# Optimization experiments

Measured on AMD Instinct MI355X. Metric: run time of the kernel, lower is better.

## Reference

```python
import jax, jax.numpy as jnp
import numpy as np

N_NODES = 100000
N_EDGES = 1600000
N_GRAPHS = 256
IN_C = 64
C = 128
N_LAYERS = 5
LN_EPS = 1e-5


def setup_inputs() -> dict:
    key = jax.random.key(0)
    ks = jax.random.split(key, 16)
    x = jax.random.normal(ks[0], (N_NODES, IN_C), dtype=jnp.float32)
    edge_index = jax.random.randint(ks[1], (2, N_EDGES), 0, N_NODES, dtype=jnp.int32)
    batch = jnp.sort(jax.random.randint(ks[2], (N_NODES,), 0, N_GRAPHS, dtype=jnp.int32))
    s_in = 1.0 / np.sqrt(IN_C)
    s_c = 1.0 / np.sqrt(C)
    s_2c = 1.0 / np.sqrt(2 * C)
    return {
        "x": x,
        "edge_index": edge_index,
        "batch": batch,
        "proj_w": jax.random.uniform(ks[3], (IN_C, C), jnp.float32, -s_in, s_in),
        "proj_b": jax.random.uniform(ks[4], (C,), jnp.float32, -s_in, s_in),
        "gin_w1": jax.random.uniform(ks[5], (N_LAYERS, C, C), jnp.float32, -s_c, s_c),
        "gin_b1": jax.random.uniform(ks[6], (N_LAYERS, C), jnp.float32, -s_c, s_c),
        "gin_w2": jax.random.uniform(ks[7], (N_LAYERS, C, C), jnp.float32, -s_c, s_c),
        "gin_b2": jax.random.uniform(ks[8], (N_LAYERS, C), jnp.float32, -s_c, s_c),
        "ln_g": jnp.ones((N_LAYERS, C), jnp.float32),
        "ln_b": jnp.zeros((N_LAYERS, C), jnp.float32),
        "fw1": jax.random.uniform(ks[9], (C, 2 * C), jnp.float32, -s_c, s_c),
        "fb1": jax.random.uniform(ks[10], (2 * C,), jnp.float32, -s_c, s_c),
        "fw2": jax.random.uniform(ks[11], (2 * C, C), jnp.float32, -s_2c, s_2c),
        "fb2": jax.random.uniform(ks[12], (C,), jnp.float32, -s_2c, s_2c),
    }


def _layer_norm(h, g, b):
    mu = jnp.mean(h, axis=-1, keepdims=True)
    var = jnp.mean(jnp.square(h - mu), axis=-1, keepdims=True)
    return (h - mu) * jax.lax.rsqrt(var + LN_EPS) * g + b


def reference(x, edge_index, batch, proj_w, proj_b, gin_w1, gin_b1, gin_w2, gin_b2,
              ln_g, ln_b, fw1, fb1, fw2, fb2):
    src, dst = edge_index[0], edge_index[1]
    h = x @ proj_w + proj_b  # [N, C]
    for i in range(N_LAYERS):
        # GINConv (eps=0): mlp(x_i + sum_{j in N(i)} x_j)
        aggr = jax.ops.segment_sum(h[src], dst, num_segments=N_NODES)  # [N, C]
        z = h + aggr
        z = jax.nn.relu(z @ gin_w1[i] + gin_b1[i]) @ gin_w2[i] + gin_b2[i]
        h = _layer_norm(jax.nn.relu(z), ln_g[i], ln_b[i])
    # global add pool over graphs
    g = jax.ops.segment_sum(h, batch, num_segments=N_GRAPHS)  # [G, C]
    out = jax.nn.relu(g @ fw1 + fb1) @ fw2 + fb2  # [G, C]
    return out
```

## Files before the change

kernel.cpp:

```cpp
#include <hip/hip_runtime.h>
#include <hip/hip_bf16.h>

#define N_NODES  100000
#define N_EDGES  1600000
#define N_GRAPHS 256
#define CCH      128
#define INC      64
#define N_LAYERS 5
#define SLICE_N  12500
#define POOL_SPLIT 16
#define CAP_A    16
#define CAP_B    32
#define CAP      (CAP_A + CAP_B)

typedef __attribute__((ext_vector_type(8))) short  short8;
typedef __attribute__((ext_vector_type(4))) float  f32x4;

__device__ __forceinline__ float bits2f(unsigned int u){ union{unsigned int i; float f;} v; v.i=u; return v.f; }
__device__ __forceinline__ float b2f(unsigned short u){ return bits2f(((unsigned int)u)<<16); }
__device__ __forceinline__ float lo16(unsigned int u){ return bits2f(u<<16); }
__device__ __forceinline__ float hi16(unsigned int u){ return bits2f(u & 0xffff0000u); }
__device__ __forceinline__ unsigned short f2b(float f){
  union{float f; unsigned int i;} v; v.f=f;
  unsigned int r = v.i + 0x7fffu + ((v.i>>16)&1u);
  return (unsigned short)(r>>16);
}
#define ACC8(a, r) { a[0]+=lo16(r.x); a[1]+=hi16(r.x); a[2]+=lo16(r.y); a[3]+=hi16(r.y); \
                     a[4]+=lo16(r.z); a[5]+=hi16(r.z); a[6]+=lo16(r.w); a[7]+=hi16(r.w); }

__global__ void pack_kernel(const float* __restrict__ projw,
                            const float* __restrict__ w1,
                            const float* __restrict__ w2,
                            unsigned short* __restrict__ wp)
{
  int idx = blockIdx.x*256 + threadIdx.x;
  const float* src; int rem;
  if (idx < 8192) { src = projw; rem = idx; }
  else {
    int t2 = idx - 8192;
    int mat = t2 >> 14;
    rem = t2 & 16383;
    src = (mat < 5) ? (w1 + mat*16384) : (w2 + (mat-5)*16384);
  }
  int f    = rem >> 9;
  int lane = (rem >> 3) & 63;
  int j    = rem & 7;
  int kk = f >> 3, nn = f & 7;
  int k = kk*32 + (lane>>4)*8 + j;
  int n = nn*16 + (lane&15);
  wp[idx] = f2b(src[k*CCH + n]);
}

__global__ __launch_bounds__(256) void fill_kernel(const int* __restrict__ src, const int* __restrict__ dst,
                                                   int* __restrict__ cnt,
                                                   int* __restrict__ esrcA, int* __restrict__ esrcB){
  int slice = blockIdx.x & 7;
  int lo = slice * SLICE_N, hi = lo + SLICE_N;
  int stride = (gridDim.x >> 3) * 256;
  for (int e = (blockIdx.x>>3)*256 + threadIdx.x; e < N_EDGES; e += stride){
    int d = __builtin_nontemporal_load(&dst[e]);
    if (d >= lo && d < hi){
      int s = __builtin_nontemporal_load(&src[e]);
      int p = atomicAdd(&cnt[d], 1);
      if (p < CAP_A)      esrcA[(size_t)d*CAP_A + p] = s;
      else if (p < CAP)   esrcB[(size_t)d*CAP_B + (p - CAP_A)] = s;
    }
  }
}

__global__ void bsearch_kernel(const int* __restrict__ batch, int* __restrict__ gstart){
  int g = threadIdx.x;
  int lo = 0, hi = N_NODES;
  while (lo < hi){
    int mid = (lo + hi) >> 1;
    if (batch[mid] < g) lo = mid + 1; else hi = mid;
  }
  gstart[g] = lo;
  if (g == 255) gstart[256] = N_NODES;
}

__global__ __launch_bounds__(256) void aggr_kernel(const unsigned short* __restrict__ h,
                                                   const int* __restrict__ cnt,
                                                   const int* __restrict__ esrcA,
                                                   const int* __restrict__ esrcB,
                                                   unsigned short* __restrict__ z)
{
  int node = blockIdx.x*4 + (threadIdx.x>>6);
  int lane = threadIdx.x & 63;
  int s = lane >> 4, c = lane & 15;
  const uint4* h16 = (const uint4*)h;
  float a[8];
  if (s == 0){
    uint4 v = h16[(size_t)node*16 + c];
    a[0]=lo16(v.x); a[1]=hi16(v.x); a[2]=lo16(v.y); a[3]=hi16(v.y);
    a[4]=lo16(v.z); a[5]=hi16(v.z); a[6]=lo16(v.w); a[7]=hi16(v.w);
  } else {
    #pragma unroll
    for (int k=0;k<8;k++) a[k] = 0.f;
  }
  int n = cnt[node]; if (n > CAP) n = CAP;
  const int* epA = esrcA + (size_t)node*CAP_A;
  const int* epB = esrcB + (size_t)node*CAP_B;

  int e = s;
  uint4 r0, r1;
  bool p0 = e < n;
  bool p1 = (e + 4) < n;
  if (p0){
    int sn = (e < CAP_A) ? epA[e] : epB[e - CAP_A];
    r0 = h16[(size_t)sn*16 + c];
  }
  if (p1){
    int e1 = e + 4;
    int sn = (e1 < CAP_A) ? epA[e1] : epB[e1 - CAP_A];
    r1 = h16[(size_t)sn*16 + c];
  }
  while (p0){
    uint4 r2; bool p2 = (e + 8) < n;
    if (p2){
      int e2 = e + 8;
      int sn = (e2 < CAP_A) ? epA[e2] : epB[e2 - CAP_A];
      r2 = h16[(size_t)sn*16 + c];
    }
    ACC8(a, r0);
    r0 = r1; p0 = p1;
    r1 = r2; p1 = p2;
    e += 4;
  }

  #pragma unroll
  for (int k=0;k<8;k++){
    a[k] += __shfl_xor(a[k], 16, 64);
    a[k] += __shfl_xor(a[k], 32, 64);
  }
  if (s == 0){
    uint4 o;
    o.x = (unsigned int)f2b(a[0]) | ((unsigned int)f2b(a[1])<<16);
    o.y = (unsigned int)f2b(a[2]) | ((unsigned int)f2b(a[3])<<16);
    o.z = (unsigned int)f2b(a[4]) | ((unsigned int)f2b(a[5])<<16);
    o.w = (unsigned int)f2b(a[6]) | ((unsigned int)f2b(a[7])<<16);
    ((uint4*)z)[(size_t)node*16 + c] = o;
  }
}

__global__ __launch_bounds__(256) void projgemm_kernel(
    const float* __restrict__ X,
    const unsigned short* __restrict__ Wp,
    const float* __restrict__ bias,
    unsigned short* __restrict__ out,
    int M)
{
  const int tid = threadIdx.x;
  const int wave = tid>>6, lane = tid&63;
  const int rbase = blockIdx.x*128 + wave*32;
  if (rbase >= M) return;
  const int cl = lane & 15, rg = lane >> 4;
  const bool ok1 = (rbase + 16) < M;

  f32x4 acc[2][8];
  #pragma unroll
  for (int s=0;s<2;s++)
    #pragma unroll
    for (int nn=0;nn<8;nn++) acc[s][nn] = (f32x4){0.f,0.f,0.f,0.f};

  const short8* wp8 = (const short8*)Wp;
  #pragma unroll
  for (int kk=0;kk<2;kk++){
    short8 bfr[8];
    #pragma unroll
    for (int nn=0;nn<8;nn++) bfr[nn] = wp8[(kk*8+nn)*64 + lane];
    #pragma unroll
    for (int s=0;s<2;s++){
      if (s==1 && !ok1) break;
      const float* xp = X + (size_t)(rbase + s*16 + cl)*INC + kk*32 + rg*8;
      float4 v0 = *(const float4*)xp;
      float4 v1 = *(const float4*)(xp+4);
      short8 af;
      af[0]=(short)f2b(v0.x); af[1]=(short)f2b(v0.y); af[2]=(short)f2b(v0.z); af[3]=(short)f2b(v0.w);
      af[4]=(short)f2b(v1.x); af[5]=(short)f2b(v1.y); af[6]=(short)f2b(v1.z); af[7]=(short)f2b(v1.w);
      #pragma unroll
      for (int nn=0;nn<8;nn++)
        acc[s][nn] = __builtin_amdgcn_mfma_f32_16x16x32_bf16(af, bfr[nn], acc[s][nn],0,0,0);
    }
  }

  float bc[8];
  #pragma unroll
  for (int nn=0;nn<8;nn++) bc[nn] = bias[nn*16+cl];

  #pragma unroll
  for (int s=0;s<2;s++){
    if (s==1 && !ok1) break;
    const int rowb = rbase + s*16 + rg*4;
    #pragma unroll
    for (int j=0;j<4;j++){
      unsigned short* op = out + (size_t)(rowb+j)*CCH + cl;
      #pragma unroll
      for (int nn=0;nn<8;nn++) op[nn*16] = f2b(acc[s][nn][j] + bc[nn]);
    }
  }
}

__global__ __launch_bounds__(256) void gemm12_kernel(
    const unsigned short* __restrict__ A,
    const unsigned short* __restrict__ Wp1,
    const float* __restrict__ b1,
    const unsigned short* __restrict__ Wp2,
    const float* __restrict__ b2,
    const float* __restrict__ lng,
    const float* __restrict__ lnb,
    unsigned short* __restrict__ out, int M)
{
  __shared__ unsigned short tl[4][32][136];
  const int tid = threadIdx.x;
  const int wave = tid>>6, lane = tid&63;
  const int rbase = blockIdx.x*128 + wave*32;
  if (rbase >= M) return;
  const int cl = lane & 15, rg = lane >> 4;
  const bool ok1 = (rbase + 16) < M;

  {
    f32x4 acc[2][8];
    #pragma unroll
    for (int s=0;s<2;s++)
      #pragma unroll
      for (int nn=0;nn<8;nn++) acc[s][nn] = (f32x4){0.f,0.f,0.f,0.f};

    const short8* wp8 = (const short8*)Wp1;
    #pragma unroll
    for (int kk=0;kk<4;kk++){
      short8 bfr[8];
      #pragma unroll
      for (int nn=0;nn<8;nn++) bfr[nn] = wp8[(kk*8+nn)*64 + lane];
      const unsigned short* ap = A + (size_t)(rbase+cl)*CCH + kk*32 + rg*8;
      short8 a0 = *(const short8*)ap;
      #pragma unroll
      for (int nn=0;nn<8;nn++)
        acc[0][nn] = __builtin_amdgcn_mfma_f32_16x16x32_bf16(a0, bfr[nn], acc[0][nn],0,0,0);
      if (ok1){
        short8 a1 = *(const short8*)(ap + (size_t)16*CCH);
        #pragma unroll
        for (int nn=0;nn<8;nn++)
          acc[1][nn] = __builtin_amdgcn_mfma_f32_16x16x32_bf16(a1, bfr[nn], acc[1][nn],0,0,0);
      }
    }
    float bc[8];
    #pragma unroll
    for (int nn=0;nn<8;nn++) bc[nn] = b1[nn*16+cl];
    #pragma unroll
    for (int s=0;s<2;s++){
      if (s==1 && !ok1) break;
      #pragma unroll
      for (int j=0;j<4;j++){
        int rel = s*16 + rg*4 + j;
        #pragma unroll
        for (int nn=0;nn<8;nn++){
          float t = acc[s][nn][j] + bc[nn];
          tl[wave][rel][nn*16+cl] = f2b(fmaxf(t, 0.f));
        }
      }
    }
  }
  {
    f32x4 acc[2][8];
    #pragma unroll
    for (int s=0;s<2;s++)
      #pragma unroll
      for (int nn=0;nn<8;nn++) acc[s][nn] = (f32x4){0.f,0.f,0.f,0.f};

    const short8* wp8 = (const short8*)Wp2;
    #pragma unroll
    for (int kk=0;kk<4;kk++){
      short8 bfr[8];
      #pragma unroll
      for (int nn=0;nn<8;nn++) bfr[nn] = wp8[(kk*8+nn)*64 + lane];
      short8 a0 = *(const short8*)&tl[wave][cl][kk*32 + rg*8];
      #pragma unroll
      for (int nn=0;nn<8;nn++)
        acc[0][nn] = __builtin_amdgcn_mfma_f32_16x16x32_bf16(a0, bfr[nn], acc[0][nn],0,0,0);
      if (ok1){
        short8 a1 = *(const short8*)&tl[wave][16+cl][kk*32 + rg*8];
        #pragma unroll
        for (int nn=0;nn<8;nn++)
          acc[1][nn] = __builtin_amdgcn_mfma_f32_16x16x32_bf16(a1, bfr[nn], acc[1][nn],0,0,0);
      }
    }
    float bc[8], gg[8], bb[8];
    #pragma unroll
    for (int nn=0;nn<8;nn++){
      bc[nn] = b2[nn*16+cl];
      gg[nn] = lng[nn*16+cl];
      bb[nn] = lnb[nn*16+cl];
    }
    #pragma unroll
    for (int s=0;s<2;s++){
      if (s==1 && !ok1) break;
      float v[8][4];
      #pragma unroll
      for (int nn=0;nn<8;nn++)
        #pragma unroll
        for (int j=0;j<4;j++)
          v[nn][j] = fmaxf(acc[s][nn][j] + bc[nn], 0.f);
      #pragma unroll
      for (int j=0;j<4;j++){
        float sm=0.f, sq=0.f;
        #pragma unroll
        for (int nn=0;nn<8;nn++){ sm += v[nn][j]; sq += v[nn][j]*v[nn][j]; }
        #pragma unroll
        for (int m=1;m<16;m<<=1){ sm += __shfl_xor(sm, m, 64); sq += __shfl_xor(sq, m, 64); }
        float mean = sm * (1.f/128.f);
        float var  = fmaxf(sq * (1.f/128.f) - mean*mean, 0.f);
        float rs = rsqrtf(var + 1e-5f);
        #pragma unroll
        for (int nn=0;nn<8;nn++) v[nn][j] = (v[nn][j]-mean)*rs*gg[nn] + bb[nn];
      }
      const int rowb = rbase + s*16 + rg*4;
      #pragma unroll
      for (int j=0;j<4;j++){
        unsigned short* op = out + (size_t)(rowb+j)*CCH + cl;
        #pragma unroll
        for (int nn=0;nn<8;nn++) op[nn*16] = f2b(v[nn][j]);
      }
    }
  }
}

__global__ __launch_bounds__(64) void pool1_kernel(const unsigned short* __restrict__ h,
                                                   const int* __restrict__ gstart,
                                                   float* __restrict__ gpart)
{
  int g = blockIdx.x >> 4;
  int sp = blockIdx.x & 15;
  int lane = threadIdx.x;
  int n0 = gstart[g], n1 = gstart[g+1];
  const unsigned int* hu = (const unsigned int*)h;
  float a0 = 0.f, a1 = 0.f;
  for (int n = n0 + sp; n < n1; n += POOL_SPLIT){
    unsigned int v = hu[(size_t)n*64 + lane];
    a0 += lo16(v); a1 += hi16(v);
  }
  float2* gp = (float2*)gpart;
  gp[(size_t)blockIdx.x*64 + lane] = make_float2(a0, a1);
}

__global__ __launch_bounds__(64) void pool2_kernel(const float* __restrict__ gpart,
                                                   float* __restrict__ gout)
{
  int g = blockIdx.x;
  int lane = threadIdx.x;
  const float2* gp = (const float2*)gpart;
  float a0 = 0.f, a1 = 0.f;
  #pragma unroll
  for (int sp=0; sp<POOL_SPLIT; sp++){
    float2 v = gp[((size_t)g*POOL_SPLIT + sp)*64 + lane];
    a0 += v.x; a1 += v.y;
  }
  ((float2*)gout)[(size_t)g*64 + lane] = make_float2(a0, a1);
}

__global__ __launch_bounds__(256) void final_kernel(const float* __restrict__ gout,
                                                    const float* __restrict__ fw1,
                                                    const float* __restrict__ fb1,
                                                    const float* __restrict__ fw2,
                                                    const float* __restrict__ fb2,
                                                    float* __restrict__ out)
{
  __shared__ float gr[128];
  __shared__ float hid[256];
  int g = blockIdx.x, t = threadIdx.x;
  if (t < 128) gr[t] = gout[g*CCH + t];
  __syncthreads();
  float a = 0.f;
  for (int k=0;k<128;k++) a += gr[k] * fw1[k*256 + t];
  a += fb1[t];
  hid[t] = fmaxf(a, 0.f);
  __syncthreads();
  if (t < 128){
    float o = 0.f;
    for (int j=0;j<256;j++) o += hid[j] * fw2[j*128 + t];
    o += fb2[t];
    out[(size_t)g*CCH + t] = o;
  }
}

extern "C" void kernel_launch(void* const* d_in, const int* in_sizes, int n_in,
                              void* d_out, int out_size, void* d_ws, size_t ws_size,
                              hipStream_t stream)
{
  const float* x     = (const float*)d_in[0];
  const int*   eidx  = (const int*)d_in[1];
  const int*   batch = (const int*)d_in[2];
  const float* projw = (const float*)d_in[3];
  const float* projb = (const float*)d_in[4];
  const float* gw1   = (const float*)d_in[5];
  const float* gb1   = (const float*)d_in[6];
  const float* gw2   = (const float*)d_in[7];
  const float* gb2   = (const float*)d_in[8];
  const float* lng   = (const float*)d_in[9];
  const float* lnb   = (const float*)d_in[10];
  const float* fw1   = (const float*)d_in[11];
  const float* fb1   = (const float*)d_in[12];
  const float* fw2   = (const float*)d_in[13];
  const float* fb2   = (const float*)d_in[14];

  const int* esrc_in = eidx;
  const int* edst_in = eidx + N_EDGES;

  char* w = (char*)d_ws; size_t off = 0;
  auto wsalloc = [&](size_t b)->char*{ char* p = w + off; off += (b + 255) & ~(size_t)255; return p; };
  unsigned short* Wp   = (unsigned short*)wsalloc(172032ull*2);
  unsigned short* h    = (unsigned short*)wsalloc((size_t)N_NODES*CCH*2);
  unsigned short* z    = (unsigned short*)wsalloc((size_t)N_NODES*CCH*2);
  int*   cnt    = (int*)wsalloc((size_t)N_NODES*4);
  int*   esrcA  = (int*)wsalloc((size_t)N_NODES*CAP_A*4);
  int*   esrcB  = (int*)wsalloc((size_t)N_NODES*CAP_B*4);
  int*   gstart = (int*)wsalloc((N_GRAPHS+1)*4);
  float* gpart  = (float*)wsalloc((size_t)N_GRAPHS*POOL_SPLIT*CCH*4);
  float* gout   = (float*)wsalloc((size_t)N_GRAPHS*CCH*4);

  hipMemsetAsync(cnt, 0, (size_t)N_NODES*4, stream);

  pack_kernel<<<672, 256, 0, stream>>>(projw, gw1, gw2, Wp);
  fill_kernel<<<2000, 256, 0, stream>>>(esrc_in, edst_in, cnt, esrcA, esrcB);
  bsearch_kernel<<<1, 256, 0, stream>>>(batch, gstart);

  projgemm_kernel<<<782, 256, 0, stream>>>(x, Wp, projb, h, N_NODES);

  for (int L=0; L<N_LAYERS; ++L){
    aggr_kernel<<<25000, 256, 0, stream>>>(h, cnt, esrcA, esrcB, z);
    gemm12_kernel<<<782, 256, 0, stream>>>(z, Wp + 8192 + L*16384, gb1 + L*CCH,
                                           Wp + 8192 + (5+L)*16384, gb2 + L*CCH,
                                           lng + L*CCH, lnb + L*CCH, h, N_NODES);
  }

  pool1_kernel<<<N_GRAPHS*POOL_SPLIT, 64, 0, stream>>>(h, gstart, gpart);
  pool2_kernel<<<N_GRAPHS, 64, 0, stream>>>(gpart, gout);
  final_kernel<<<N_GRAPHS, 256, 0, stream>>>(gout, fw1, fb1, fw2, fb2, (float*)d_out);
}
```

Baseline: 576.8 us.

## Partition edges into destination slices before filling adjacency lists

Replaces the single fill pass, in which every block scans all edges and keeps only those for its slice, with two passes. A partition kernel buckets the (src,dst) pairs into 8 destination-slice buffers using block-local shared atomics, and a fill kernel then reads only its slice's edges to build the per-node lists. This cuts the 8x redundant reading of the dst array, at the cost of an extra kernel launch and a write and read of an 8-byte-per-edge staging buffer. Each slice buffer has a fixed capacity, so edges beyond it would be silently dropped if a slice overflowed.

```diff
diff --git a/kernel.cpp b/kernel.cpp
--- a/kernel.cpp
+++ b/kernel.cpp
@@ -12,6 +12,7 @@
 #define CAP_A    16
 #define CAP_B    32
 #define CAP      (CAP_A + CAP_B)
+#define EB_CAP   220000
 
 typedef __attribute__((ext_vector_type(8))) short  short8;
 typedef __attribute__((ext_vector_type(4))) float  f32x4;
@@ -51,20 +52,59 @@
   wp[idx] = f2b(src[k*CCH + n]);
 }
 
-__global__ __launch_bounds__(256) void fill_kernel(const int* __restrict__ src, const int* __restrict__ dst,
-                                                   int* __restrict__ cnt,
-                                                   int* __restrict__ esrcA, int* __restrict__ esrcB){
+__global__ void init_kernel(int* __restrict__ bcur){
+  if (threadIdx.x < 8) bcur[threadIdx.x] = threadIdx.x * EB_CAP;
+}
+
+__global__ __launch_bounds__(256) void part_kernel(const int* __restrict__ src,
+                                                   const int* __restrict__ dst,
+                                                   int* __restrict__ bcur,
+                                                   int2* __restrict__ ebuf){
+  __shared__ int lcnt[8];
+  __shared__ int lbase[8];
+  int tid = threadIdx.x;
+  if (tid < 8) lcnt[tid] = 0;
+  __syncthreads();
+  int e0 = blockIdx.x * 2048;
+  int ds[8], ss[8];
+  #pragma unroll
+  for (int i = 0; i < 8; i++){
+    int e = e0 + i*256 + tid;
+    if (e < N_EDGES){
+      ds[i] = dst[e]; ss[i] = src[e];
+      atomicAdd(&lcnt[ds[i]/SLICE_N], 1);
+    } else ds[i] = -1;
+  }
+  __syncthreads();
+  if (tid < 8){
+    lbase[tid] = atomicAdd(&bcur[tid], lcnt[tid]);
+    lcnt[tid] = 0;
+  }
+  __syncthreads();
+  #pragma unroll
+  for (int i = 0; i < 8; i++){
+    if (ds[i] >= 0){
+      int b = ds[i]/SLICE_N;
+      int p = lbase[b] + atomicAdd(&lcnt[b], 1);
+      if (p < (b+1)*EB_CAP) ebuf[p] = make_int2(ss[i], ds[i]);
+    }
+  }
+}
+
+__global__ __launch_bounds__(256) void fill2_kernel(const int2* __restrict__ ebuf,
+                                                    const int* __restrict__ bcur,
+                                                    int* __restrict__ cnt,
+                                                    int* __restrict__ esrcA, int* __restrict__ esrcB){
   int slice = blockIdx.x & 7;
-  int lo = slice * SLICE_N, hi = lo + SLICE_N;
+  int start = slice * EB_CAP;
+  int end   = bcur[slice]; if (end > start + EB_CAP) end = start + EB_CAP;
   int stride = (gridDim.x >> 3) * 256;
-  for (int e = (blockIdx.x>>3)*256 + threadIdx.x; e < N_EDGES; e += stride){
-    int d = __builtin_nontemporal_load(&dst[e]);
-    if (d >= lo && d < hi){
-      int s = __builtin_nontemporal_load(&src[e]);
-      int p = atomicAdd(&cnt[d], 1);
-      if (p < CAP_A)      esrcA[(size_t)d*CAP_A + p] = s;
-      else if (p < CAP)   esrcB[(size_t)d*CAP_B + (p - CAP_A)] = s;
-    }
+  for (int i = start + (blockIdx.x>>3)*256 + threadIdx.x; i < end; i += stride){
+    int2 e = ebuf[i];
+    int d = e.y;
+    int p = atomicAdd(&cnt[d], 1);
+    if (p < CAP_A)      esrcA[(size_t)d*CAP_A + p] = e.x;
+    else if (p < CAP)   esrcB[(size_t)d*CAP_B + (p - CAP_A)] = e.x;
   }
 }
 
@@ -414,14 +454,18 @@
   int*   cnt    = (int*)wsalloc((size_t)N_NODES*4);
   int*   esrcA  = (int*)wsalloc((size_t)N_NODES*CAP_A*4);
   int*   esrcB  = (int*)wsalloc((size_t)N_NODES*CAP_B*4);
+  int*   bcur   = (int*)wsalloc(256);
+  int2*  ebuf   = (int2*)wsalloc((size_t)8*EB_CAP*8);
   int*   gstart = (int*)wsalloc((N_GRAPHS+1)*4);
   float* gpart  = (float*)wsalloc((size_t)N_GRAPHS*POOL_SPLIT*CCH*4);
   float* gout   = (float*)wsalloc((size_t)N_GRAPHS*CCH*4);
 
   hipMemsetAsync(cnt, 0, (size_t)N_NODES*4, stream);
 
+  init_kernel<<<1, 64, 0, stream>>>(bcur);
   pack_kernel<<<672, 256, 0, stream>>>(projw, gw1, gw2, Wp);
-  fill_kernel<<<2000, 256, 0, stream>>>(esrc_in, edst_in, cnt, esrcA, esrcB);
+  part_kernel<<<782, 256, 0, stream>>>(esrc_in, edst_in, bcur, ebuf);
+  fill2_kernel<<<2000, 256, 0, stream>>>(ebuf, bcur, cnt, esrcA, esrcB);
   bsearch_kernel<<<1, 256, 0, stream>>>(batch, gstart);
 
   projgemm_kernel<<<782, 256, 0, stream>>>(x, Wp, projb, h, N_NODES);
```

New measurement: 589.2 us. 2.1% more time.
